# Kernel tuning notes

Hardware: AMD Instinct MI355X
Metric: run time of the kernel (lower is better)

The kernel has to match this reference:

```python
import jax, jax.numpy as jnp
import numpy as np

SEQ, BATCH, HID, NLAYERS = 2048, 16, 1024, 2


def setup_inputs() -> dict:
    key = jax.random.key(0)
    ks = jax.random.split(key, 3)
    scale = 1.0 / np.sqrt(HID)
    x = jax.random.normal(ks[0], (SEQ, BATCH, HID), dtype=jnp.float32)
    W0 = jax.random.normal(ks[1], (HID, 3 * HID), dtype=jnp.float32) * scale
    b0 = jnp.zeros((2 * HID,), dtype=jnp.float32)
    W1 = jax.random.normal(ks[2], (HID, 3 * HID), dtype=jnp.float32) * scale
    b1 = jnp.zeros((2 * HID,), dtype=jnp.float32)
    return {"x": x, "W0": W0, "b0": b0, "W1": W1, "b1": b1}


def _sru_layer(x, W, b):
    # x: [L, B, H]; W: [H, 3H]; b: [2H]
    L, B, H = x.shape
    U = jnp.einsum('lbd,dk->lbk', x, W)  # [L, B, 3H]
    x_tilde = U[..., :H]
    bf, br = b[:H], b[H:]
    f = jax.nn.sigmoid(U[..., H:2 * H] + bf)  # forget gate [L,B,H]
    r = jax.nn.sigmoid(U[..., 2 * H:] + br)   # reset gate  [L,B,H]

    def step(c_prev, inp):
        xt_t, f_t = inp
        c_t = f_t * c_prev + (1.0 - f_t) * xt_t
        return c_t, c_t

    c0 = jnp.zeros((B, H), dtype=x.dtype)
    _, cs = jax.lax.scan(step, c0, (x_tilde, f))  # cs: [L, B, H]
    h = r * cs + (1.0 - r) * x  # highway connection
    return h


def reference(x, W0, b0, W1, b1):
    h = _sru_layer(x, W0, b0)
    h = _sru_layer(h, W1, b1)
    return h[-1:]  # [1, B, H], matching `out[-1:]`
```

## Files before the change

kernel.cpp:

```cpp
#include <hip/hip_runtime.h>

#define SEQ    2048
#define BATCH  16
#define HID    1024
#define M_TOT  (SEQ*BATCH)
#define NCH    (BATCH*HID)
#define NCHUNK 32
#define TCHUNK (SEQ/NCHUNK)

typedef __attribute__((ext_vector_type(8))) short          short8;
typedef __attribute__((ext_vector_type(8))) unsigned short ushort8_t;
typedef __attribute__((ext_vector_type(4))) float          floatx4;

__device__ __forceinline__ unsigned short f32_to_bf16(float f) {
  unsigned int u = __float_as_uint(f);
  u += 0x7FFFu + ((u >> 16) & 1u);
  return (unsigned short)(u >> 16);
}
__device__ __forceinline__ float bf16_to_f32(unsigned short h) {
  return __uint_as_float(((unsigned int)h) << 16);
}
__device__ __forceinline__ float sigmoidf_(float x) {
  return 1.f / (1.f + __expf(-x));
}

#define LDS_DMA16(gp, lp) \
  __builtin_amdgcn_global_load_lds((const __attribute__((address_space(1))) void*)(gp), \
                                   (__attribute__((address_space(3))) void*)(lp), 16, 0, 0)


__device__ __forceinline__ void cast_swizzle_body(const float* __restrict__ src,
    unsigned short* __restrict__ dst, int mt, int kt, int t) {
  __shared__ unsigned short tile[4096];
  const int r = t >> 1, kh = (t & 1) * 16;
  const float* sp = src + (size_t)(mt * 128 + r) * 1024 + kt * 32 + kh;
  float4 v0 = *(const float4*)(sp + 0);
  float4 v1 = *(const float4*)(sp + 4);
  float4 v2 = *(const float4*)(sp + 8);
  float4 v3 = *(const float4*)(sp + 12);
  ushort8_t u0, u1;
  u0[0]=f32_to_bf16(v0.x); u0[1]=f32_to_bf16(v0.y); u0[2]=f32_to_bf16(v0.z); u0[3]=f32_to_bf16(v0.w);
  u0[4]=f32_to_bf16(v1.x); u0[5]=f32_to_bf16(v1.y); u0[6]=f32_to_bf16(v1.z); u0[7]=f32_to_bf16(v1.w);
  u1[0]=f32_to_bf16(v2.x); u1[1]=f32_to_bf16(v2.y); u1[2]=f32_to_bf16(v2.z); u1[3]=f32_to_bf16(v2.w);
  u1[4]=f32_to_bf16(v3.x); u1[5]=f32_to_bf16(v3.y); u1[6]=f32_to_bf16(v3.z); u1[7]=f32_to_bf16(v3.w);
  const int c = r >> 4, lr = r & 15, q0 = kh >> 3;
  const int unit0 = c * 64 + (q0 << 4) + lr;
  *(ushort8_t*)&tile[unit0 * 8]        = u0;
  *(ushort8_t*)&tile[(unit0 + 16) * 8] = u1;
  __syncthreads();
  const size_t base = ((size_t)mt * 32 + kt) * 4096;
  *(ushort8_t*)&dst[base + t * 16]     = *(const ushort8_t*)&tile[t * 16];
  *(ushort8_t*)&dst[base + t * 16 + 8] = *(const ushort8_t*)&tile[t * 16 + 8];
}

__device__ __forceinline__ void w_prep_body(const float* __restrict__ W,
    unsigned short* __restrict__ Wsw, int nt, int kt, int t) {
  __shared__ unsigned short tile[4096];
  const int kk = t >> 3, n0 = (t & 7) * 16;
  const float* sp = W + (size_t)(kt * 32 + kk) * 3072 + nt * 128 + n0;
  float v[16];
#pragma unroll
  for (int i = 0; i < 16; i += 4) {
    float4 f = *(const float4*)(sp + i);
    v[i] = f.x; v[i+1] = f.y; v[i+2] = f.z; v[i+3] = f.w;
  }
  const int cbase = (n0 >> 4) * 64 + ((kk >> 3) << 4);
#pragma unroll
  for (int j = 0; j < 16; j++)
    tile[(cbase + j) * 8 + (kk & 7)] = f32_to_bf16(v[j]);
  __syncthreads();
  const size_t base = ((size_t)nt * 32 + kt) * 4096;
  *(ushort8_t*)&Wsw[base + t * 16]     = *(const ushort8_t*)&tile[t * 16];
  *(ushort8_t*)&Wsw[base + t * 16 + 8] = *(const ushort8_t*)&tile[t * 16 + 8];
}

__global__ __launch_bounds__(256) void prep_all(const float* __restrict__ x,
    const float* __restrict__ W0, const float* __restrict__ W1,
    unsigned short* __restrict__ xsw, unsigned short* __restrict__ W0sw,
    unsigned short* __restrict__ W1sw) {
  const int id = blockIdx.x, t = threadIdx.x;
  if (id < 8192)        cast_swizzle_body(x, xsw, id >> 5, id & 31, t);
  else if (id < 8960)   w_prep_body(W0, W0sw, (id - 8192) >> 5, (id - 8192) & 31, t);
  else                  w_prep_body(W1, W1sw, (id - 8960) >> 5, (id - 8960) & 31, t);
}

__global__ __launch_bounds__(256, 4) void gemm_sw_fused(
    const unsigned short* __restrict__ A, const unsigned short* __restrict__ B,
    unsigned short* __restrict__ Xt, unsigned short* __restrict__ Fo, unsigned short* __restrict__ Ro,
    const float* __restrict__ bias, int NBN)
{
  __shared__ __align__(16) unsigned short As[2][4096];
  __shared__ __align__(16) unsigned short Bs[2][4096];
  const int tid = threadIdx.x;
  const int wave = tid >> 6, lane = tid & 63;
  const int id = blockIdx.x;
  const int xcd = id & 7, slot = id >> 3;
  const int NB8 = NBN << 3;
  const int g    = slot / NB8;
  const int rem  = slot - g * NB8;
  const int bn   = rem >> 3;
  const int bm   = xcd * 32 + g * 8 + (rem & 7);
  const int wm = wave >> 1, wn = wave & 1;

  const int so = wave * 1024 + lane * 8;
  const unsigned short* gA = A + (size_t)bm * 32 * 4096 + so;
  const unsigned short* gB = B + (size_t)bn * 32 * 4096 + so;
  const int l0 = wave * 1024;

  floatx4 acc[4][4];
#pragma unroll
  for (int i = 0; i < 4; i++)
#pragma unroll
    for (int j = 0; j < 4; j++)
#pragma unroll
      for (int r = 0; r < 4; r++) acc[i][j][r] = 0.f;

  const int ra = wm * 2048 + lane * 8;
  const int rb = wn * 2048 + lane * 8;

  auto stage = [&](int buf) {
    LDS_DMA16(gA,       As[buf] + l0);
    LDS_DMA16(gA + 512, As[buf] + l0 + 512);
    LDS_DMA16(gB,       Bs[buf] + l0);
    LDS_DMA16(gB + 512, Bs[buf] + l0 + 512);
    gA += 4096; gB += 4096;
  };
  auto compute = [&](int buf) {
    short8 a[4], b[4];
#pragma unroll
    for (int i = 0; i < 4; i++) a[i] = *(const short8*)(As[buf] + ra + i * 512);
#pragma unroll
    for (int j = 0; j < 4; j++) b[j] = *(const short8*)(Bs[buf] + rb + j * 512);
#pragma unroll
    for (int i = 0; i < 4; i++)
#pragma unroll
      for (int j = 0; j < 4; j++)
        acc[i][j] = __builtin_amdgcn_mfma_f32_16x16x32_bf16(a[i], b[j], acc[i][j], 0, 0, 0);
  };

  stage(0);
#pragma unroll 1
  for (int kt = 0; kt < 32; kt += 2) {
    __syncthreads();
    stage(1);
    compute(0);
    __syncthreads();
    if (kt + 2 < 32) stage(0);
    compute(1);
  }

  const int region = bn >> 3;
  const int colb = (bn & 7) * 128 + wn * 64 + (lane & 15);
  const int row0 = bm * 128 + wm * 64 + ((lane >> 4) << 2);
  if (region == 0) {
#pragma unroll
    for (int i = 0; i < 4; i++)
#pragma unroll
      for (int j = 0; j < 4; j++)
#pragma unroll
        for (int rg = 0; rg < 4; rg++)
          Xt[(size_t)(row0 + i * 16 + rg) * 1024 + colb + j * 16] = f32_to_bf16(acc[i][j][rg]);
  } else {
    unsigned short* O = (region == 1) ? Fo : Ro;
    const float* bp = bias + (region - 1) * 1024;
#pragma unroll
    for (int j = 0; j < 4; j++) {
      float bb = bp[colb + j * 16];
#pragma unroll
      for (int i = 0; i < 4; i++)
#pragma unroll
        for (int rg = 0; rg < 4; rg++) {
          float s = sigmoidf_(acc[i][j][rg] + bb);
          O[(size_t)(row0 + i * 16 + rg) * 1024 + colb + j * 16] = f32_to_bf16(s);
        }
    }
  }
}

__global__ __launch_bounds__(256) void scan_pass1(
    const unsigned short* __restrict__ Xt, const unsigned short* __restrict__ F,
    float* __restrict__ P, float* __restrict__ S) {
  const int ch = (blockIdx.x * 256 + threadIdx.x) * 8;
  const int chunk = blockIdx.y;
  size_t idx = (size_t)chunk * TCHUNK * NCH + ch;
  float p[8], s[8];
#pragma unroll
  for (int j = 0; j < 8; j++) { p[j] = 1.f; s[j] = 0.f; }
  for (int t = 0; t < TCHUNK; ++t) {
    ushort8_t fv = *(const ushort8_t*)&F[idx];
    ushort8_t xv = *(const ushort8_t*)&Xt[idx];
#pragma unroll
    for (int j = 0; j < 8; j++) {
      float f  = bf16_to_f32(fv[j]);
      float xt = bf16_to_f32(xv[j]);
      s[j] = f * s[j] + (1.f - f) * xt;
      p[j] *= f;
    }
    idx += NCH;
  }
  float4* P4 = (float4*)&P[(size_t)chunk * NCH + ch];
  float4* S4 = (float4*)&S[(size_t)chunk * NCH + ch];
  P4[0] = make_float4(p[0], p[1], p[2], p[3]);
  P4[1] = make_float4(p[4], p[5], p[6], p[7]);
  S4[0] = make_float4(s[0], s[1], s[2], s[3]);
  S4[1] = make_float4(s[4], s[5], s[6], s[7]);
}

__global__ __launch_bounds__(256) void combine_c0(
    const float* __restrict__ P, const float* __restrict__ S, float* __restrict__ C0) {
  const int ch = (blockIdx.x * 256 + threadIdx.x) * 8;
  float c[8];
#pragma unroll
  for (int j = 0; j < 8; j++) c[j] = 0.f;
  for (int k = 0; k < NCHUNK; ++k) {
    float4* O4 = (float4*)&C0[(size_t)k * NCH + ch];
    O4[0] = make_float4(c[0], c[1], c[2], c[3]);
    O4[1] = make_float4(c[4], c[5], c[6], c[7]);
    const float4* P4 = (const float4*)&P[(size_t)k * NCH + ch];
    const float4* S4 = (const float4*)&S[(size_t)k * NCH + ch];
    float4 p0 = P4[0], p1 = P4[1], s0 = S4[0], s1 = S4[1];
    c[0] = p0.x*c[0]+s0.x; c[1] = p0.y*c[1]+s0.y; c[2] = p0.z*c[2]+s0.z; c[3] = p0.w*c[3]+s0.w;
    c[4] = p1.x*c[4]+s1.x; c[5] = p1.y*c[5]+s1.y; c[6] = p1.z*c[6]+s1.z; c[7] = p1.w*c[7]+s1.w;
  }
}

#define TPAD 4112
__global__ __launch_bounds__(256) void scan1_pass2_fused(
    const unsigned short* __restrict__ Xt, const unsigned short* __restrict__ F,
    const unsigned short* __restrict__ R, const unsigned short* __restrict__ xsw,
    const float* __restrict__ C0, unsigned short* __restrict__ h1sw,
    unsigned short* __restrict__ h1last)
{
  __shared__ unsigned short st[4 * TPAD];
  const int hb = blockIdx.x;
  const int chunk = blockIdx.y;
  const int tid = threadIdx.x;
  const int b = tid >> 4, hg = tid & 15;
  const int h0 = hb * 128 + hg * 8;
  const int ch = b * 1024 + h0;
  const int tl   = hg >> 2;
  const int usub = (hg & 3) * 16 + b;

  float c[8];
  {
    const float4* C4 = (const float4*)&C0[(size_t)chunk * NCH + ch];
    float4 a = C4[0], d = C4[1];
    c[0]=a.x; c[1]=a.y; c[2]=a.z; c[3]=a.w; c[4]=d.x; c[5]=d.y; c[6]=d.z; c[7]=d.w;
  }

  size_t idx = (size_t)chunk * TCHUNK * NCH + ch;
  for (int t8 = 0; t8 < 8; ++t8) {
#pragma unroll
    for (int ts = 0; ts < 8; ++ts) {
      const int t = chunk * TCHUNK + t8 * 8 + ts;
      ushort8_t fv = *(const ushort8_t*)&F[idx];
      ushort8_t xv = *(const ushort8_t*)&Xt[idx];
      ushort8_t rv = *(const ushort8_t*)&R[idx];
      const size_t soff = ((size_t)(t >> 3) * 32 + (h0 >> 5)) * 4096
                        + (size_t)(((t & 7) * 64 + usub) * 8);
      ushort8_t xo = *(const ushort8_t*)&xsw[soff];
      ushort8_t hv;
#pragma unroll
      for (int j = 0; j < 8; ++j) {
        float f  = bf16_to_f32(fv[j]);
        float xt = bf16_to_f32(xv[j]);
        c[j] = f * c[j] + (1.f - f) * xt;
        float r  = bf16_to_f32(rv[j]);
        float xval = bf16_to_f32(xo[j]);
        hv[j] = f32_to_bf16(r * c[j] + (1.f - r) * xval);
      }
      *(ushort8_t*)&st[tl * TPAD + (ts * 64 + usub) * 8] = hv;
      if (t == SEQ - 1) *(ushort8_t*)&h1last[ch] = hv;
      idx += NCH;
    }
    __syncthreads();
    const size_t gbase = (((size_t)chunk * 8 + t8) * 32 + hb * 4) * 4096;
#pragma unroll
    for (int tl2 = 0; tl2 < 4; ++tl2) {
      size_t gdst = gbase + (size_t)tl2 * 4096 + tid * 16;
      *(ushort8_t*)&h1sw[gdst]     = *(const ushort8_t*)&st[tl2 * TPAD + tid * 16];
      *(ushort8_t*)&h1sw[gdst + 8] = *(const ushort8_t*)&st[tl2 * TPAD + tid * 16 + 8];
    }
    __syncthreads();
  }
}

__global__ __launch_bounds__(256) void r2_kernel(
    const unsigned short* __restrict__ h1last, const float* __restrict__ W1,
    const float* __restrict__ b1, float* __restrict__ r2) {
  __shared__ float xrow[1024];
  const int b = blockIdx.x, nq = blockIdx.y, tid = threadIdx.x;
  for (int i = tid; i < 1024; i += 256)
    xrow[i] = bf16_to_f32(h1last[b * 1024 + i]);
  __syncthreads();
  const int n = nq * 256 + tid;
  float acc = b1[1024 + n];
  for (int d = 0; d < 1024; ++d)
    acc += xrow[d] * W1[(size_t)d * 3072 + 2048 + n];
  r2[b * 1024 + n] = sigmoidf_(acc);
}

__global__ __launch_bounds__(256) void combine_final(
    const float* __restrict__ P, const float* __restrict__ S,
    const float* __restrict__ r2, const unsigned short* __restrict__ h1last,
    float* __restrict__ out) {
  const int ch = (blockIdx.x * 256 + threadIdx.x) * 8;
  float c[8];
#pragma unroll
  for (int j = 0; j < 8; j++) c[j] = 0.f;
  for (int k = 0; k < NCHUNK; ++k) {
    const float4* P4 = (const float4*)&P[(size_t)k * NCH + ch];
    const float4* S4 = (const float4*)&S[(size_t)k * NCH + ch];
    float4 p0 = P4[0], p1 = P4[1], s0 = S4[0], s1 = S4[1];
    c[0] = p0.x*c[0]+s0.x; c[1] = p0.y*c[1]+s0.y; c[2] = p0.z*c[2]+s0.z; c[3] = p0.w*c[3]+s0.w;
    c[4] = p1.x*c[4]+s1.x; c[5] = p1.y*c[5]+s1.y; c[6] = p1.z*c[6]+s1.z; c[7] = p1.w*c[7]+s1.w;
  }
  const float4* R4 = (const float4*)&r2[ch];
  float4 r0 = R4[0], r1 = R4[1];
  ushort8_t hx = *(const ushort8_t*)&h1last[ch];
  float o[8];
  float rr[8] = {r0.x, r0.y, r0.z, r0.w, r1.x, r1.y, r1.z, r1.w};
#pragma unroll
  for (int j = 0; j < 8; j++)
    o[j] = rr[j] * c[j] + (1.f - rr[j]) * bf16_to_f32(hx[j]);
  float4* O4 = (float4*)&out[ch];
  O4[0] = make_float4(o[0], o[1], o[2], o[3]);
  O4[1] = make_float4(o[4], o[5], o[6], o[7]);
}

extern "C" void kernel_launch(void* const* d_in, const int* in_sizes, int n_in,
                              void* d_out, int out_size, void* d_ws, size_t ws_size,
                              hipStream_t stream) {
  const float* x  = (const float*)d_in[0];
  const float* W0 = (const float*)d_in[1];
  const float* b0 = (const float*)d_in[2];
  const float* W1 = (const float*)d_in[3];
  const float* b1 = (const float*)d_in[4];
  float* out = (float*)d_out;

  char* ws = (char*)d_ws;
  auto alloc = [&](size_t bytes) {
    char* p = ws; ws += (bytes + 255) & ~(size_t)255; return p;
  };
  const size_t NE = (size_t)M_TOT * HID;
  unsigned short* xsw   = (unsigned short*)alloc(NE * 2);
  unsigned short* W0sw  = (unsigned short*)alloc((size_t)3072 * 1024 * 2);
  unsigned short* W1sw  = (unsigned short*)alloc((size_t)3072 * 1024 * 2);
  unsigned short* Xt    = (unsigned short*)alloc(NE * 2);
  unsigned short* F     = (unsigned short*)alloc(NE * 2);
  unsigned short* R     = (unsigned short*)alloc(NE * 2);
  unsigned short* h1sw  = (unsigned short*)alloc(NE * 2);
  unsigned short* h1last= (unsigned short*)alloc((size_t)NCH * 2);
  float* P   = (float*)alloc((size_t)NCHUNK * NCH * 4);
  float* S   = (float*)alloc((size_t)NCHUNK * NCH * 4);
  float* C0  = (float*)alloc((size_t)NCHUNK * NCH * 4);
  float* r2  = (float*)alloc((size_t)NCH * 4);

  dim3 blk256(256);
  prep_all<<<dim3(9728), blk256, 0, stream>>>(x, W0, W1, xsw, W0sw, W1sw);
  gemm_sw_fused<<<dim3(24 * 256), blk256, 0, stream>>>(xsw, W0sw, Xt, F, R, b0, 24);
  scan_pass1<<<dim3(8, NCHUNK), blk256, 0, stream>>>(Xt, F, P, S);
  combine_c0<<<dim3(8), blk256, 0, stream>>>(P, S, C0);
  scan1_pass2_fused<<<dim3(8, NCHUNK), blk256, 0, stream>>>(Xt, F, R, xsw, C0, h1sw, h1last);
  gemm_sw_fused<<<dim3(16 * 256), blk256, 0, stream>>>(h1sw, W1sw, Xt, F, R, b1, 16);
  r2_kernel<<<dim3(16, 4), blk256, 0, stream>>>(h1last, W1, b1, r2);
  scan_pass1<<<dim3(8, NCHUNK), blk256, 0, stream>>>(Xt, F, P, S);
  combine_final<<<dim3(8), blk256, 0, stream>>>(P, S, r2, h1last, out);
}
```

Before: 843.4 us.

## Replace LDS-staged GEMM with direct register-loaded 128x256 tiles and reuse xsw buffer

The GEMM no longer stages tiles through LDS with DMA and barriers. Each wave now loads its pre-swizzled A and B fragments straight from global memory into registers, double-buffered in registers. The block tile grows to 128x256, with each wave computing 64x128 and occupancy hint lowered to 2. The layer-1 scan output is written in place into the xsw buffer, so the separate h1sw allocation goes away. This removes LDS traffic and synchronisation, at the cost of duplicated global/L2 loads across waves, more register pressure, and reliance on in-place overwrite ordering.

```diff
diff --git a/kernel.cpp b/kernel.cpp
--- a/kernel.cpp
+++ b/kernel.cpp
@@ -23,10 +23,6 @@
 __device__ __forceinline__ float sigmoidf_(float x) {
   return 1.f / (1.f + __expf(-x));
 }
-
-#define LDS_DMA16(gp, lp) \
-  __builtin_amdgcn_global_load_lds((const __attribute__((address_space(1))) void*)(gp), \
-                                   (__attribute__((address_space(3))) void*)(lp), 16, 0, 0)
 
 
 __device__ __forceinline__ void cast_swizzle_body(const float* __restrict__ src,
@@ -84,94 +80,82 @@
   else                  w_prep_body(W1, W1sw, (id - 8960) >> 5, (id - 8960) & 31, t);
 }
 
-__global__ __launch_bounds__(256, 4) void gemm_sw_fused(
+__global__ __launch_bounds__(256, 2) void gemm_direct(
     const unsigned short* __restrict__ A, const unsigned short* __restrict__ B,
     unsigned short* __restrict__ Xt, unsigned short* __restrict__ Fo, unsigned short* __restrict__ Ro,
-    const float* __restrict__ bias, int NBN)
+    const float* __restrict__ bias, int NBN2)
 {
-  __shared__ __align__(16) unsigned short As[2][4096];
-  __shared__ __align__(16) unsigned short Bs[2][4096];
   const int tid = threadIdx.x;
   const int wave = tid >> 6, lane = tid & 63;
+  const int wm = wave & 1, wn = wave >> 1;
   const int id = blockIdx.x;
   const int xcd = id & 7, slot = id >> 3;
-  const int NB8 = NBN << 3;
-  const int g    = slot / NB8;
-  const int rem  = slot - g * NB8;
-  const int bn   = rem >> 3;
-  const int bm   = xcd * 32 + g * 8 + (rem & 7);
-  const int wm = wave >> 1, wn = wave & 1;
-
-  const int so = wave * 1024 + lane * 8;
-  const unsigned short* gA = A + (size_t)bm * 32 * 4096 + so;
-  const unsigned short* gB = B + (size_t)bn * 32 * 4096 + so;
-  const int l0 = wave * 1024;
-
-  floatx4 acc[4][4];
+  const int NB8 = NBN2 << 3;
+  const int g = slot / NB8, rem = slot - g * NB8;
+  const int bn = rem >> 3;
+  const int bm = xcd * 32 + g * 8 + (rem & 7);
+
+  const unsigned short* gA = A + (size_t)bm * 32 * 4096 + wm * 2048 + lane * 8;
+  const unsigned short* gB = B + ((size_t)(bn * 2 + wn)) * 32 * 4096 + lane * 8;
+
+  floatx4 acc[4][8];
 #pragma unroll
   for (int i = 0; i < 4; i++)
 #pragma unroll
-    for (int j = 0; j < 4; j++)
+    for (int j = 0; j < 8; j++)
 #pragma unroll
       for (int r = 0; r < 4; r++) acc[i][j][r] = 0.f;
 
-  const int ra = wm * 2048 + lane * 8;
-  const int rb = wn * 2048 + lane * 8;
-
-  auto stage = [&](int buf) {
-    LDS_DMA16(gA,       As[buf] + l0);
-    LDS_DMA16(gA + 512, As[buf] + l0 + 512);
-    LDS_DMA16(gB,       Bs[buf] + l0);
-    LDS_DMA16(gB + 512, Bs[buf] + l0 + 512);
-    gA += 4096; gB += 4096;
+  short8 a0[4], b0[8], a1[4], b1[8];
+  auto loadA = [&](short8* d, const unsigned short* p) {
+#pragma unroll
+    for (int i = 0; i < 4; i++) d[i] = *(const short8*)(p + i * 512);
   };
-  auto compute = [&](int buf) {
-    short8 a[4], b[4];
-#pragma unroll
-    for (int i = 0; i < 4; i++) a[i] = *(const short8*)(As[buf] + ra + i * 512);
-#pragma unroll
-    for (int j = 0; j < 4; j++) b[j] = *(const short8*)(Bs[buf] + rb + j * 512);
+  auto loadB = [&](short8* d, const unsigned short* p) {
+#pragma unroll
+    for (int j = 0; j < 8; j++) d[j] = *(const short8*)(p + j * 512);
+  };
+  auto domfma = [&](short8* a, short8* b) {
 #pragma unroll
     for (int i = 0; i < 4; i++)
 #pragma unroll
-      for (int j = 0; j < 4; j++)
+      for (int j = 0; j < 8; j++)
         acc[i][j] = __builtin_amdgcn_mfma_f32_16x16x32_bf16(a[i], b[j], acc[i][j], 0, 0, 0);
   };
 
-  stage(0);
+  loadA(a0, gA); loadB(b0, gB);
 #pragma unroll 1
   for (int kt = 0; kt < 32; kt += 2) {
-    __syncthreads();
-    stage(1);
-    compute(0);
-    __syncthreads();
-    if (kt + 2 < 32) stage(0);
-    compute(1);
-  }
-
-  const int region = bn >> 3;
-  const int colb = (bn & 7) * 128 + wn * 64 + (lane & 15);
+    loadA(a1, gA + 4096); loadB(b1, gB + 4096);
+    domfma(a0, b0);
+    gA += 8192; gB += 8192;
+    if (kt + 2 < 32) { loadA(a0, gA); loadB(b0, gB); }
+    domfma(a1, b1);
+  }
+
+  const int region = bn >> 2;
+  const int lc = (bn & 3) * 256 + wn * 128 + (lane & 15);
   const int row0 = bm * 128 + wm * 64 + ((lane >> 4) << 2);
   if (region == 0) {
 #pragma unroll
     for (int i = 0; i < 4; i++)
 #pragma unroll
-      for (int j = 0; j < 4; j++)
+      for (int j = 0; j < 8; j++)
 #pragma unroll
         for (int rg = 0; rg < 4; rg++)
-          Xt[(size_t)(row0 + i * 16 + rg) * 1024 + colb + j * 16] = f32_to_bf16(acc[i][j][rg]);
+          Xt[(size_t)(row0 + i * 16 + rg) * 1024 + lc + j * 16] = f32_to_bf16(acc[i][j][rg]);
   } else {
     unsigned short* O = (region == 1) ? Fo : Ro;
     const float* bp = bias + (region - 1) * 1024;
 #pragma unroll
-    for (int j = 0; j < 4; j++) {
-      float bb = bp[colb + j * 16];
+    for (int j = 0; j < 8; j++) {
+      float bb = bp[lc + j * 16];
 #pragma unroll
       for (int i = 0; i < 4; i++)
 #pragma unroll
         for (int rg = 0; rg < 4; rg++) {
           float s = sigmoidf_(acc[i][j][rg] + bb);
-          O[(size_t)(row0 + i * 16 + rg) * 1024 + colb + j * 16] = f32_to_bf16(s);
+          O[(size_t)(row0 + i * 16 + rg) * 1024 + lc + j * 16] = f32_to_bf16(s);
         }
     }
   }
@@ -227,9 +211,8 @@
 #define TPAD 4112
 __global__ __launch_bounds__(256) void scan1_pass2_fused(
     const unsigned short* __restrict__ Xt, const unsigned short* __restrict__ F,
-    const unsigned short* __restrict__ R, const unsigned short* __restrict__ xsw,
-    const float* __restrict__ C0, unsigned short* __restrict__ h1sw,
-    unsigned short* __restrict__ h1last)
+    const unsigned short* __restrict__ R, unsigned short* __restrict__ xsw,
+    const float* __restrict__ C0, unsigned short* __restrict__ h1last)
 {
   __shared__ unsigned short st[4 * TPAD];
   const int hb = blockIdx.x;
@@ -278,8 +261,8 @@
 #pragma unroll
     for (int tl2 = 0; tl2 < 4; ++tl2) {
       size_t gdst = gbase + (size_t)tl2 * 4096 + tid * 16;
-      *(ushort8_t*)&h1sw[gdst]     = *(const ushort8_t*)&st[tl2 * TPAD + tid * 16];
-      *(ushort8_t*)&h1sw[gdst + 8] = *(const ushort8_t*)&st[tl2 * TPAD + tid * 16 + 8];
+      *(ushort8_t*)&xsw[gdst]     = *(const ushort8_t*)&st[tl2 * TPAD + tid * 16];
+      *(ushort8_t*)&xsw[gdst + 8] = *(const ushort8_t*)&st[tl2 * TPAD + tid * 16 + 8];
     }
     __syncthreads();
   }
@@ -349,7 +332,6 @@
   unsigned short* Xt    = (unsigned short*)alloc(NE * 2);
   unsigned short* F     = (unsigned short*)alloc(NE * 2);
   unsigned short* R     = (unsigned short*)alloc(NE * 2);
-  unsigned short* h1sw  = (unsigned short*)alloc(NE * 2);
   unsigned short* h1last= (unsigned short*)alloc((size_t)NCH * 2);
   float* P   = (float*)alloc((size_t)NCHUNK * NCH * 4);
   float* S   = (float*)alloc((size_t)NCHUNK * NCH * 4);
@@ -358,11 +340,11 @@
 
   dim3 blk256(256);
   prep_all<<<dim3(9728), blk256, 0, stream>>>(x, W0, W1, xsw, W0sw, W1sw);
-  gemm_sw_fused<<<dim3(24 * 256), blk256, 0, stream>>>(xsw, W0sw, Xt, F, R, b0, 24);
+  gemm_direct<<<dim3(256 * 12), blk256, 0, stream>>>(xsw, W0sw, Xt, F, R, b0, 12);
   scan_pass1<<<dim3(8, NCHUNK), blk256, 0, stream>>>(Xt, F, P, S);
   combine_c0<<<dim3(8), blk256, 0, stream>>>(P, S, C0);
-  scan1_pass2_fused<<<dim3(8, NCHUNK), blk256, 0, stream>>>(Xt, F, R, xsw, C0, h1sw, h1last);
-  gemm_sw_fused<<<dim3(16 * 256), blk256, 0, stream>>>(h1sw, W1sw, Xt, F, R, b1, 16);
+  scan1_pass2_fused<<<dim3(8, NCHUNK), blk256, 0, stream>>>(Xt, F, R, xsw, C0, h1last);
+  gemm_direct<<<dim3(256 * 8), blk256, 0, stream>>>(xsw, W1sw, Xt, F, R, b1, 8);
   r2_kernel<<<dim3(16, 4), blk256, 0, stream>>>(h1last, W1, b1, r2);
   scan_pass1<<<dim3(8, NCHUNK), blk256, 0, stream>>>(Xt, F, P, S);
   combine_final<<<dim3(8), blk256, 0, stream>>>(P, S, r2, h1last, out);
```

After: 833.9 us. No clear change (-1.1%).
